# Performance work log

Hardware: AMD Instinct MI355X
Metric: run time of the kernel (lower is better)

Reference implementation:

```python
import jax, jax.numpy as jnp
import numpy as np

N = 500000
EMB = 256
CONT = {0: [0, 1, 4, 6, 7, 8, 9, 10, 11, 12, 13],
        1: [0, 1, 4, 5, 6, 7, 8, 9, 10, 11, 12, 13],
        2: [1, 2, 4, 5, 6, 7, 8, 9, 10, 11, 12, 13],
        3: [2, 3, 4, 5, 6, 7, 8, 9, 10, 11, 12, 13]}
DISC = {0: [2, 3, 5], 1: [2, 3], 2: [0], 3: [0, 1]}
DIMS = {0: {2: 96, 3: 8, 5: 2}, 1: {2: 4, 3: 22}, 2: {0: 6}, 3: {0: 15, 1: 96}}


def _splits(n):
    # emb_dim split across n discrete features, remainder to the first ones
    per, r = EMB // n, EMB % n
    return [per + (1 if i < r else 0) for i in range(n)]


def setup_inputs() -> dict:
    key = jax.random.key(0)
    x = jax.random.normal(jax.random.fold_in(key, 0), (N, 14), jnp.float32)
    # discrete columns must hold valid integer codes for every node type using them
    col_max = {0: 6, 1: 96, 2: 4, 3: 8, 5: 2}
    for c, m in col_max.items():
        v = jax.random.randint(jax.random.fold_in(key, 100 + c), (N,), 0, m)
        x = x.at[:, c].set(v.astype(jnp.float32))
    node_types = jax.random.randint(jax.random.fold_in(key, 1), (N,), 0, 4)
    inp = {"x": x, "node_types": node_types}
    for t in range(4):
        fan_in = len(CONT[t])
        s = float(np.sqrt(6.0 / (fan_in + EMB)))  # xavier_uniform bound
        inp[f"W{t}"] = jax.random.uniform(jax.random.fold_in(key, 10 + t), (EMB, fan_in), jnp.float32, -s, s)
        inp[f"b{t}"] = jax.random.uniform(jax.random.fold_in(key, 20 + t), (EMB,), jnp.float32, -0.05, 0.05)
        dims = _splits(len(DISC[t]))
        for i, c in enumerate(DISC[t]):
            vocab = DIMS[t][c]
            se = float(np.sqrt(6.0 / (vocab + dims[i])))
            inp[f"E{t}_{c}"] = jax.random.uniform(jax.random.fold_in(key, 1000 + 10 * t + c), (vocab, dims[i]), jnp.float32, -se, se)
    return inp


def _forward(x, node_types, Ws, bs, Es):
    out = jnp.zeros((x.shape[0], EMB), x.dtype)
    for t in range(4):  # fixed small set of node types (static MoE dispatch)
        mask = node_types == t  # [N]
        # discrete embeddings: gather per feature column, concat to [N, EMB]
        disc = jnp.concatenate(
            [Es[t][i][x[:, c].astype(jnp.int32)] for i, c in enumerate(DISC[t])], axis=1)
        # continuous projection: [N, in_dim] @ [in_dim, EMB] + bias
        cont = x[:, jnp.array(CONT[t])] @ Ws[t].T + bs[t]
        out = jnp.where(mask[:, None], disc + cont, out)
    return out


def reference(x, node_types, W0, b0, W1, b1, W2, b2, W3, b3,
              E0_2, E0_3, E0_5, E1_2, E1_3, E2_0, E3_0, E3_1):
    Ws = [W0, W1, W2, W3]
    bs = [b0, b1, b2, b3]
    Es = {0: [E0_2, E0_3, E0_5], 1: [E1_2, E1_3], 2: [E2_0], 3: [E3_0, E3_1]}
    return _forward(x, node_types, Ws, bs, Es)
```

## Files before the change

### kernel.cpp

```cpp
#include <hip/hip_runtime.h>

typedef float fvec4 __attribute__((ext_vector_type(4)));
typedef unsigned short ushort_t;

#define NBLK 256
#define TPB  1024
#define NG   16
#define CN   512

#define LAUNDER_PTR(p) asm volatile("" : "+v"(p))

#define O_E0_2 0
#define O_E0_3 8450
#define O_E0_5 9155
#define O_E1_2 9332
#define O_E1_3 9844
#define O_E2_0 12660
#define O_E3_0 14196
#define O_E3_1 16116
#define NTAB   28404
#define XSH    NTAB
#define IDXF   (XSH + CN * 16)
#define CNTI   (IDXF + 2048)
#define SMEM_FLOATS (CNTI + 8)
#define SMEM_BYTES  (SMEM_FLOATS * 4)

extern __shared__ float smem[];

#define FMA4(K, XV)                                   \
    acc.x = fmaf(w[0][K], (XV), acc.x);               \
    acc.y = fmaf(w[1][K], (XV), acc.y);               \
    acc.z = fmaf(w[2][K], (XV), acc.z);               \
    acc.w = fmaf(w[3][K], (XV), acc.w);

__global__ __launch_bounds__(TPB, 1)
void node_enc_kernel(const float* __restrict__ x,
                     const int* __restrict__ node_types,
                     const float* __restrict__ W0, const float* __restrict__ b0,
                     const float* __restrict__ E0_2, const float* __restrict__ E0_3,
                     const float* __restrict__ E0_5,
                     const float* __restrict__ W1, const float* __restrict__ b1,
                     const float* __restrict__ E1_2, const float* __restrict__ E1_3,
                     const float* __restrict__ W2, const float* __restrict__ b2,
                     const float* __restrict__ E2_0,
                     const float* __restrict__ W3, const float* __restrict__ b3,
                     const float* __restrict__ E3_0, const float* __restrict__ E3_1,
                     float* __restrict__ out, int n_nodes)
{
    const int tid = threadIdx.x;
    const int q   = tid & 63;
    const int h   = tid >> 6;

    auto copy_tab = [&](const float* __restrict__ src, int dst, int n) {
        if ((((uintptr_t)src) & 15) == 0) {
            const int nv = n >> 2;
            for (int i = tid; i < nv; i += TPB) {
                const fvec4 v = *(reinterpret_cast<const fvec4*>(src) + i);
                *reinterpret_cast<fvec4*>(&smem[dst + (i << 2)]) = v;
            }
            for (int i = (nv << 2) + tid; i < n; i += TPB) smem[dst + i] = src[i];
        } else {
            for (int i = tid; i < n; i += TPB) smem[dst + i] = src[i];
        }
    };
    auto copy_tab_pad = [&](const float* __restrict__ src, int dst, int rows, int cols) {
        const int n = rows * cols;
        for (int i = tid; i < n; i += TPB) {
            const int r = i / cols, c2 = i - r * cols;
            smem[dst + r * 88 + c2] = src[i];
        }
    };
    copy_tab_pad(E0_2, O_E0_2, 96, 86);
    copy_tab_pad(E0_3, O_E0_3, 8, 85);
    copy_tab_pad(E0_5, O_E0_5, 2, 85);
    copy_tab(E1_2, O_E1_2, 512);
    copy_tab(E1_3, O_E1_3, 2816);
    copy_tab(E2_0, O_E2_0, 1536);
    copy_tab(E3_0, O_E3_0, 1920);
    copy_tab(E3_1, O_E3_1, 12288);

    const int nch = (n_nodes + CN - 1) / CN;
    const int c0  = (int)(((long long)blockIdx.x * nch) / NBLK);
    const int c1  = (int)(((long long)(blockIdx.x + 1) * nch) / NBLK);

    ushort_t* const idx_m = reinterpret_cast<ushort_t*>(&smem[IDXF]);
    int*      const cnt_m = reinterpret_cast<int*>(&smem[CNTI]);
    const ushort_t* idx_ro = idx_m;
    const int*      cnt_ro = cnt_m;

    auto stage_issue = [&](int c, fvec4& r0, fvec4& r1,
                           float& rs, int& ty, int& nv, int& total, int& cnn) {
        const long long cb = (long long)c * CN;
        cnn   = min(CN, (int)(n_nodes - cb));
        total = cnn * 14;
        nv    = total >> 2;
        const fvec4* vsrc = reinterpret_cast<const fvec4*>(x + cb * 14);
        if (tid < nv)          r0 = __builtin_nontemporal_load(vsrc + tid);
        if (tid + TPB < nv)    r1 = __builtin_nontemporal_load(vsrc + tid + TPB);
        const int sf = (nv << 2) + tid;
        if (sf < total) rs = x[cb * 14 + sf];
        if (tid < cnn)  ty = node_types[cb + tid];
    };
    auto stage_write = [&](const fvec4& r0, const fvec4& r1,
                           float rs, int nv, int total) {
        auto wr1 = [&](int i, const fvec4& v) {
            const int f = i << 2;
            int node = f / 14, col = f - node * 14;
            #pragma unroll
            for (int j = 0; j < 4; ++j) {
                smem[XSH + node * 16 + col] = v[j];
                if (++col == 14) { col = 0; ++node; }
            }
        };
        if (tid < nv)        wr1(tid, r0);
        if (tid + TPB < nv)  wr1(tid + TPB, r1);
        const int sf = (nv << 2) + tid;
        if (sf < total) { const int node = sf / 14, col = sf - node * 14; smem[XSH + node * 16 + col] = rs; }
    };

    auto do_chunk = [&](int c, int p) {
        const long long cb = (long long)c * CN;
        const int cbase = p * 4;
        const int ibase = p * 2048;

        {
            const int m = cnt_ro[cbase + 0];
            const float* Wp = W0; LAUNDER_PTR(Wp);
            const float* bp = b0; LAUNDER_PTR(bp);
            float w[4][11];
            #pragma unroll
            for (int j = 0; j < 4; ++j) {
                #pragma unroll
                for (int k = 0; k < 11; ++k) w[j][k] = Wp[(4 * q + j) * 11 + k];
            }
            float4 bias;
            bias.x = bp[4 * q]; bias.y = bp[4 * q + 1];
            bias.z = bp[4 * q + 2]; bias.w = bp[4 * q + 3];
            int scv, ebase;
            const bool fb = (q == 21) || (q == 42);
            if (q <= 21)      { scv = 2; ebase = O_E0_2 + 4 * q; }
            else if (q <= 42) { scv = 3; ebase = (O_E0_3 - 86) + 4 * q; }
            else              { scv = 5; ebase = (O_E0_5 - 171) + 4 * q; }
            for (int g = h; g < m; g += NG) {
                const int nl = idx_ro[ibase + 0 * CN + g];
                const float* xr = &smem[XSH + nl * 16];
                const float4 ra = *reinterpret_cast<const float4*>(xr);
                const float4 rb = *reinterpret_cast<const float4*>(xr + 4);
                const float4 rc = *reinterpret_cast<const float4*>(xr + 8);
                const float2 rd = *reinterpret_cast<const float2*>(xr + 12);
                float4 acc = bias;
                FMA4(0,  ra.x) FMA4(1,  ra.y) FMA4(2,  rb.x) FMA4(3,  rb.z)
                FMA4(4,  rb.w) FMA4(5,  rc.x) FMA4(6,  rc.y) FMA4(7,  rc.z)
                FMA4(8,  rc.w) FMA4(9,  rd.x) FMA4(10, rd.y)
                float4 ev;
                if (fb) {
                    if (q == 21) {
                        const int c2 = (int)xr[2], c3 = (int)xr[3];
                        ev.x = smem[O_E0_2 + c2 * 88 + 84];
                        ev.y = smem[O_E0_2 + c2 * 88 + 85];
                        ev.z = smem[O_E0_3 + c3 * 88 + 0];
                        ev.w = smem[O_E0_3 + c3 * 88 + 1];
                    } else {
                        const int c3 = (int)xr[3], c5 = (int)xr[5];
                        ev.x = smem[O_E0_3 + c3 * 88 + 82];
                        ev.y = smem[O_E0_3 + c3 * 88 + 83];
                        ev.z = smem[O_E0_3 + c3 * 88 + 84];
                        ev.w = smem[O_E0_5 + c5 * 88 + 0];
                    }
                } else {
                    const int code = (int)xr[scv];
                    ev = *reinterpret_cast<const float4*>(&smem[ebase + code * 88]);
                }
                acc.x += ev.x; acc.y += ev.y; acc.z += ev.z; acc.w += ev.w;
                *reinterpret_cast<float4*>(&out[(cb + nl) * 256 + 4 * q]) = acc;
            }
        }

        {
            const int m = cnt_ro[cbase + 1];
            const float* Wp = W1; LAUNDER_PTR(Wp);
            const float* bp = b1; LAUNDER_PTR(bp);
            float w[4][12];
            #pragma unroll
            for (int j = 0; j < 4; ++j) {
                #pragma unroll
                for (int k = 0; k < 12; ++k) w[j][k] = Wp[(4 * q + j) * 12 + k];
            }
            float4 bias;
            bias.x = bp[4 * q]; bias.y = bp[4 * q + 1];
            bias.z = bp[4 * q + 2]; bias.w = bp[4 * q + 3];
            const int scv   = (q < 32) ? 2 : 3;
            const int ebase = ((q < 32) ? O_E1_2 : (O_E1_3 - 128)) + 4 * q;
            for (int g = h; g < m; g += NG) {
                const int nl = idx_ro[ibase + 1 * CN + g];
                const float* xr = &smem[XSH + nl * 16];
                const float4 ra = *reinterpret_cast<const float4*>(xr);
                const float4 rb = *reinterpret_cast<const float4*>(xr + 4);
                const float4 rc = *reinterpret_cast<const float4*>(xr + 8);
                const float2 rd = *reinterpret_cast<const float2*>(xr + 12);
                float4 acc = bias;
                FMA4(0,  ra.x) FMA4(1,  ra.y) FMA4(2,  rb.x) FMA4(3,  rb.y)
                FMA4(4,  rb.z) FMA4(5,  rb.w) FMA4(6,  rc.x) FMA4(7,  rc.y)
                FMA4(8,  rc.z) FMA4(9,  rc.w) FMA4(10, rd.x) FMA4(11, rd.y)
                const int code = (int)xr[scv];
                const float4 ev = *reinterpret_cast<const float4*>(&smem[ebase + code * 128]);
                acc.x += ev.x; acc.y += ev.y; acc.z += ev.z; acc.w += ev.w;
                *reinterpret_cast<float4*>(&out[(cb + nl) * 256 + 4 * q]) = acc;
            }
        }

        {
            const int m = cnt_ro[cbase + 2];
            const float* Wp = W2; LAUNDER_PTR(Wp);
            const float* bp = b2; LAUNDER_PTR(bp);
            float w[4][12];
            #pragma unroll
            for (int j = 0; j < 4; ++j) {
                #pragma unroll
                for (int k = 0; k < 12; ++k) w[j][k] = Wp[(4 * q + j) * 12 + k];
            }
            float4 bias;
            bias.x = bp[4 * q]; bias.y = bp[4 * q + 1];
            bias.z = bp[4 * q + 2]; bias.w = bp[4 * q + 3];
            const int ebase = O_E2_0 + 4 * q;
            for (int g = h; g < m; g += NG) {
                const int nl = idx_ro[ibase + 2 * CN + g];
                const float* xr = &smem[XSH + nl * 16];
                const float4 ra = *reinterpret_cast<const float4*>(xr);
                const float4 rb = *reinterpret_cast<const float4*>(xr + 4);
                const float4 rc = *reinterpret_cast<const float4*>(xr + 8);
                const float2 rd = *reinterpret_cast<const float2*>(xr + 12);
                float4 acc = bias;
                FMA4(0,  ra.y) FMA4(1,  ra.z) FMA4(2,  rb.x) FMA4(3,  rb.y)
                FMA4(4,  rb.z) FMA4(5,  rb.w) FMA4(6,  rc.x) FMA4(7,  rc.y)
                FMA4(8,  rc.z) FMA4(9,  rc.w) FMA4(10, rd.x) FMA4(11, rd.y)
                const int code = (int)xr[0];
                const float4 ev = *reinterpret_cast<const float4*>(&smem[ebase + code * 256]);
                acc.x += ev.x; acc.y += ev.y; acc.z += ev.z; acc.w += ev.w;
                *reinterpret_cast<float4*>(&out[(cb + nl) * 256 + 4 * q]) = acc;
            }
        }

        {
            const int m = cnt_ro[cbase + 3];
            const float* Wp = W3; LAUNDER_PTR(Wp);
            const float* bp = b3; LAUNDER_PTR(bp);
            float w[4][12];
            #pragma unroll
            for (int j = 0; j < 4; ++j) {
                #pragma unroll
                for (int k = 0; k < 12; ++k) w[j][k] = Wp[(4 * q + j) * 12 + k];
            }
            float4 bias;
            bias.x = bp[4 * q]; bias.y = bp[4 * q + 1];
            bias.z = bp[4 * q + 2]; bias.w = bp[4 * q + 3];
            const int scv   = (q < 32) ? 0 : 1;
            const int ebase = ((q < 32) ? O_E3_0 : (O_E3_1 - 128)) + 4 * q;
            for (int g = h; g < m; g += NG) {
                const int nl = idx_ro[ibase + 3 * CN + g];
                const float* xr = &smem[XSH + nl * 16];
                const float4 ra = *reinterpret_cast<const float4*>(xr);
                const float4 rb = *reinterpret_cast<const float4*>(xr + 4);
                const float4 rc = *reinterpret_cast<const float4*>(xr + 8);
                const float2 rd = *reinterpret_cast<const float2*>(xr + 12);
                float4 acc = bias;
                FMA4(0,  ra.z) FMA4(1,  ra.w) FMA4(2,  rb.x) FMA4(3,  rb.y)
                FMA4(4,  rb.z) FMA4(5,  rb.w) FMA4(6,  rc.x) FMA4(7,  rc.y)
                FMA4(8,  rc.z) FMA4(9,  rc.w) FMA4(10, rd.x) FMA4(11, rd.y)
                const int code = (int)xr[scv];
                const float4 ev = *reinterpret_cast<const float4*>(&smem[ebase + code * 128]);
                acc.x += ev.x; acc.y += ev.y; acc.z += ev.z; acc.w += ev.w;
                *reinterpret_cast<float4*>(&out[(cb + nl) * 256 + 4 * q]) = acc;
            }
        }
    };

    {
        fvec4 r0, r1; float rs = 0.f; int ty = 0, nv = 0, total = 0, cnn = 0;
        if (c0 < c1) {
            stage_issue(c0, r0, r1, rs, ty, nv, total, cnn);
            stage_write(r0, r1, rs, nv, total);
            if (tid < 8) cnt_m[tid] = 0;
        }
        __syncthreads();
        if (c0 < c1 && tid < cnn) {
            const int p0 = atomicAdd(&cnt_m[0 + ty], 1);
            idx_m[0 + ty * CN + p0] = (ushort_t)tid;
        }
        __syncthreads();
    }

    for (int c = c0; c < c1; ++c) {
        const int p = (c - c0) & 1;
        fvec4 r0, r1; float rs = 0.f; int ty = 0, nv = 0, total = 0, cnn = 0;
        const bool hasnext = (c + 1 < c1);
        if (hasnext) {
            stage_issue(c + 1, r0, r1, rs, ty, nv, total, cnn);
            if (tid < 4) cnt_m[(p ^ 1) * 4 + tid] = 0;
        }
        do_chunk(c, p);
        __syncthreads();
        if (hasnext) {
            stage_write(r0, r1, rs, nv, total);
            if (tid < cnn) {
                const int pos = atomicAdd(&cnt_m[(p ^ 1) * 4 + ty], 1);
                idx_m[(p ^ 1) * 2048 + ty * CN + pos] = (ushort_t)tid;
            }
        }
        __syncthreads();
    }
}

extern "C" void kernel_launch(void* const* d_in, const int* in_sizes, int n_in,
                              void* d_out, int out_size, void* d_ws, size_t ws_size,
                              hipStream_t stream) {
    const float* xp   = (const float*)d_in[0];
    const int*   ntp  = (const int*)d_in[1];
    const float* W0 = (const float*)d_in[2];
    const float* b0 = (const float*)d_in[3];
    const float* E0_2 = (const float*)d_in[4];
    const float* E0_3 = (const float*)d_in[5];
    const float* E0_5 = (const float*)d_in[6];
    const float* W1 = (const float*)d_in[7];
    const float* b1 = (const float*)d_in[8];
    const float* E1_2 = (const float*)d_in[9];
    const float* E1_3 = (const float*)d_in[10];
    const float* W2 = (const float*)d_in[11];
    const float* b2 = (const float*)d_in[12];
    const float* E2_0 = (const float*)d_in[13];
    const float* W3 = (const float*)d_in[14];
    const float* b3 = (const float*)d_in[15];
    const float* E3_0 = (const float*)d_in[16];
    const float* E3_1 = (const float*)d_in[17];
    float* outp = (float*)d_out;

    const int n_nodes = in_sizes[1];

    (void)hipFuncSetAttribute(reinterpret_cast<const void*>(node_enc_kernel),
                              hipFuncAttributeMaxDynamicSharedMemorySize, SMEM_BYTES);

    node_enc_kernel<<<NBLK, TPB, SMEM_BYTES, stream>>>(
        xp, ntp, W0, b0, E0_2, E0_3, E0_5, W1, b1, E1_2, E1_3,
        W2, b2, E2_0, W3, b3, E3_0, E3_1, outp, n_nodes);
}
```

Measured before the change: 126.7 us.

## Store embedding tables as bf16 in LDS and shrink blocks for higher occupancy

Embedding tables are converted to bf16 when copied into shared memory, which roughly halves their LDS footprint. This lets the kernel run 512 threads per block with chunk size 256, 512 blocks and launch bounds allowing several blocks per CU. The intent is more latency hiding for the output-write-bound loop. The cost is reduced precision of the embedding values (bf16 rounding), which may exceed the tolerance, plus double the per-block table staging since there are twice as many blocks.

```diff
diff --git a/kernel.cpp b/kernel.cpp
--- a/kernel.cpp
+++ b/kernel.cpp
@@ -1,14 +1,22 @@
 #include <hip/hip_runtime.h>
+#include <hip/hip_bf16.h>
 
 typedef float fvec4 __attribute__((ext_vector_type(4)));
 typedef unsigned short ushort_t;
-
-#define NBLK 256
-#define TPB  1024
-#define NG   16
-#define CN   512
+typedef unsigned int uint_t;
+
+#define NBLK 512
+#define TPB  512
+#define NG   8
+#define CN   256
 
 #define LAUNDER_PTR(p) asm volatile("" : "+v"(p))
+
+#define XSH    0
+#define IDXF   4096
+#define CNTI   5120
+#define TABF   5128
+#define TABU   (TABF * 2)
 
 #define O_E0_2 0
 #define O_E0_3 8450
@@ -18,14 +26,18 @@
 #define O_E2_0 12660
 #define O_E3_0 14196
 #define O_E3_1 16116
-#define NTAB   28404
-#define XSH    NTAB
-#define IDXF   (XSH + CN * 16)
-#define CNTI   (IDXF + 2048)
-#define SMEM_FLOATS (CNTI + 8)
-#define SMEM_BYTES  (SMEM_FLOATS * 4)
+#define NTABU  28404
+#define SMEM_BYTES (TABF * 4 + NTABU * 2)
 
 extern __shared__ float smem[];
+
+__device__ __forceinline__ ushort_t f2bf(float v) {
+    __hip_bfloat16 h = __float2bfloat16(v);
+    return *reinterpret_cast<ushort_t*>(&h);
+}
+__device__ __forceinline__ float bf2f(ushort_t u) {
+    return __uint_as_float(((uint_t)u) << 16);
+}
 
 #define FMA4(K, XV)                                   \
     acc.x = fmaf(w[0][K], (XV), acc.x);               \
@@ -33,7 +45,13 @@
     acc.z = fmaf(w[2][K], (XV), acc.z);               \
     acc.w = fmaf(w[3][K], (XV), acc.w);
 
-__global__ __launch_bounds__(TPB, 1)
+#define BF4_DECODE(u, ev)                             \
+    ev.x = __uint_as_float(u.x << 16);                \
+    ev.y = __uint_as_float(u.x & 0xffff0000u);        \
+    ev.z = __uint_as_float(u.y << 16);                \
+    ev.w = __uint_as_float(u.y & 0xffff0000u);
+
+__global__ __launch_bounds__(TPB, 4)
 void node_enc_kernel(const float* __restrict__ x,
                      const int* __restrict__ node_types,
                      const float* __restrict__ W0, const float* __restrict__ b0,
@@ -51,33 +69,26 @@
     const int q   = tid & 63;
     const int h   = tid >> 6;
 
-    auto copy_tab = [&](const float* __restrict__ src, int dst, int n) {
-        if ((((uintptr_t)src) & 15) == 0) {
-            const int nv = n >> 2;
-            for (int i = tid; i < nv; i += TPB) {
-                const fvec4 v = *(reinterpret_cast<const fvec4*>(src) + i);
-                *reinterpret_cast<fvec4*>(&smem[dst + (i << 2)]) = v;
-            }
-            for (int i = (nv << 2) + tid; i < n; i += TPB) smem[dst + i] = src[i];
-        } else {
-            for (int i = tid; i < n; i += TPB) smem[dst + i] = src[i];
-        }
-    };
-    auto copy_tab_pad = [&](const float* __restrict__ src, int dst, int rows, int cols) {
+    ushort_t* const tab = reinterpret_cast<ushort_t*>(smem) + TABU;
+
+    auto copy_tab_bf = [&](const float* __restrict__ src, int dst, int n) {
+        for (int i = tid; i < n; i += TPB) tab[dst + i] = f2bf(src[i]);
+    };
+    auto copy_tab_pad_bf = [&](const float* __restrict__ src, int dst, int rows, int cols) {
         const int n = rows * cols;
         for (int i = tid; i < n; i += TPB) {
             const int r = i / cols, c2 = i - r * cols;
-            smem[dst + r * 88 + c2] = src[i];
-        }
-    };
-    copy_tab_pad(E0_2, O_E0_2, 96, 86);
-    copy_tab_pad(E0_3, O_E0_3, 8, 85);
-    copy_tab_pad(E0_5, O_E0_5, 2, 85);
-    copy_tab(E1_2, O_E1_2, 512);
-    copy_tab(E1_3, O_E1_3, 2816);
-    copy_tab(E2_0, O_E2_0, 1536);
-    copy_tab(E3_0, O_E3_0, 1920);
-    copy_tab(E3_1, O_E3_1, 12288);
+            tab[dst + r * 88 + c2] = f2bf(src[i]);
+        }
+    };
+    copy_tab_pad_bf(E0_2, O_E0_2, 96, 86);
+    copy_tab_pad_bf(E0_3, O_E0_3, 8, 85);
+    copy_tab_pad_bf(E0_5, O_E0_5, 2, 85);
+    copy_tab_bf(E1_2, O_E1_2, 512);
+    copy_tab_bf(E1_3, O_E1_3, 2816);
+    copy_tab_bf(E2_0, O_E2_0, 1536);
+    copy_tab_bf(E3_0, O_E3_0, 1920);
+    copy_tab_bf(E3_1, O_E3_1, 12288);
 
     const int nch = (n_nodes + CN - 1) / CN;
     const int c0  = (int)(((long long)blockIdx.x * nch) / NBLK);
@@ -121,7 +132,7 @@
     auto do_chunk = [&](int c, int p) {
         const long long cb = (long long)c * CN;
         const int cbase = p * 4;
-        const int ibase = p * 2048;
+        const int ibase = p * 1024;
 
         {
             const int m = cnt_ro[cbase + 0];
@@ -156,20 +167,21 @@
                 if (fb) {
                     if (q == 21) {
                         const int c2 = (int)xr[2], c3 = (int)xr[3];
-                        ev.x = smem[O_E0_2 + c2 * 88 + 84];
-                        ev.y = smem[O_E0_2 + c2 * 88 + 85];
-                        ev.z = smem[O_E0_3 + c3 * 88 + 0];
-                        ev.w = smem[O_E0_3 + c3 * 88 + 1];
+                        ev.x = bf2f(tab[O_E0_2 + c2 * 88 + 84]);
+                        ev.y = bf2f(tab[O_E0_2 + c2 * 88 + 85]);
+                        ev.z = bf2f(tab[O_E0_3 + c3 * 88 + 0]);
+                        ev.w = bf2f(tab[O_E0_3 + c3 * 88 + 1]);
                     } else {
                         const int c3 = (int)xr[3], c5 = (int)xr[5];
-                        ev.x = smem[O_E0_3 + c3 * 88 + 82];
-                        ev.y = smem[O_E0_3 + c3 * 88 + 83];
-                        ev.z = smem[O_E0_3 + c3 * 88 + 84];
-                        ev.w = smem[O_E0_5 + c5 * 88 + 0];
+                        ev.x = bf2f(tab[O_E0_3 + c3 * 88 + 82]);
+                        ev.y = bf2f(tab[O_E0_3 + c3 * 88 + 83]);
+                        ev.z = bf2f(tab[O_E0_3 + c3 * 88 + 84]);
+                        ev.w = bf2f(tab[O_E0_5 + c5 * 88 + 0]);
                     }
                 } else {
                     const int code = (int)xr[scv];
-                    ev = *reinterpret_cast<const float4*>(&smem[ebase + code * 88]);
+                    const uint2 u = *reinterpret_cast<const uint2*>(&tab[ebase + code * 88]);
+                    BF4_DECODE(u, ev)
                 }
                 acc.x += ev.x; acc.y += ev.y; acc.z += ev.z; acc.w += ev.w;
                 *reinterpret_cast<float4*>(&out[(cb + nl) * 256 + 4 * q]) = acc;
@@ -203,7 +215,9 @@
                 FMA4(4,  rb.z) FMA4(5,  rb.w) FMA4(6,  rc.x) FMA4(7,  rc.y)
                 FMA4(8,  rc.z) FMA4(9,  rc.w) FMA4(10, rd.x) FMA4(11, rd.y)
                 const int code = (int)xr[scv];
-                const float4 ev = *reinterpret_cast<const float4*>(&smem[ebase + code * 128]);
+                const uint2 u = *reinterpret_cast<const uint2*>(&tab[ebase + code * 128]);
+                float4 ev;
+                BF4_DECODE(u, ev)
                 acc.x += ev.x; acc.y += ev.y; acc.z += ev.z; acc.w += ev.w;
                 *reinterpret_cast<float4*>(&out[(cb + nl) * 256 + 4 * q]) = acc;
             }
@@ -235,7 +249,9 @@
                 FMA4(4,  rb.z) FMA4(5,  rb.w) FMA4(6,  rc.x) FMA4(7,  rc.y)
                 FMA4(8,  rc.z) FMA4(9,  rc.w) FMA4(10, rd.x) FMA4(11, rd.y)
                 const int code = (int)xr[0];
-                const float4 ev = *reinterpret_cast<const float4*>(&smem[ebase + code * 256]);
+                const uint2 u = *reinterpret_cast<const uint2*>(&tab[ebase + code * 256]);
+                float4 ev;
+                BF4_DECODE(u, ev)
                 acc.x += ev.x; acc.y += ev.y; acc.z += ev.z; acc.w += ev.w;
                 *reinterpret_cast<float4*>(&out[(cb + nl) * 256 + 4 * q]) = acc;
             }
@@ -268,7 +284,9 @@
                 FMA4(4,  rb.z) FMA4(5,  rb.w) FMA4(6,  rc.x) FMA4(7,  rc.y)
                 FMA4(8,  rc.z) FMA4(9,  rc.w) FMA4(10, rd.x) FMA4(11, rd.y)
                 const int code = (int)xr[scv];
-                const float4 ev = *reinterpret_cast<const float4*>(&smem[ebase + code * 128]);
+                const uint2 u = *reinterpret_cast<const uint2*>(&tab[ebase + code * 128]);
+                float4 ev;
+                BF4_DECODE(u, ev)
                 acc.x += ev.x; acc.y += ev.y; acc.z += ev.z; acc.w += ev.w;
                 *reinterpret_cast<float4*>(&out[(cb + nl) * 256 + 4 * q]) = acc;
             }
@@ -304,7 +322,7 @@
             stage_write(r0, r1, rs, nv, total);
             if (tid < cnn) {
                 const int pos = atomicAdd(&cnt_m[(p ^ 1) * 4 + ty], 1);
-                idx_m[(p ^ 1) * 2048 + ty * CN + pos] = (ushort_t)tid;
+                idx_m[(p ^ 1) * 1024 + ty * CN + pos] = (ushort_t)tid;
             }
         }
         __syncthreads();
```

After: 135.8 us. +7.2%, slower.
